# Kernel optimization log

Hardware: AMD Instinct MI355X
Metric: run time of the kernel (lower is better)

Reference implementation:

```python
import jax, jax.numpy as jnp
import numpy as np

N = 1024          # n noisy tokens (seq = 2*N)
DIM = 768
HEADS = 12
HD = DIM // HEADS
BLOCK = 16        # diffusion block size
COND = 128
DFF = 4 * DIM
NEG = -1e30


def rotate_half(x):
    x1, x2 = jnp.split(x, 2, axis=-1)
    return jnp.concatenate((-x2, x1), axis=-1)


def layernorm(x):
    mu = jnp.mean(x, axis=-1, keepdims=True)
    var = jnp.var(x, axis=-1, keepdims=True)
    return (x - mu) * jax.lax.rsqrt(var + 1e-5)


def block_diff_mask(seq, n, block_size):
    idx = jnp.arange(seq)
    q_idx, kv_idx = idx[:, None], idx[None, :]
    fq = q_idx >= n
    fk = kv_idx >= n
    bq = jnp.where(fq, (q_idx - n) // block_size, q_idx // block_size)
    bk = jnp.where(fk, (kv_idx - n) // block_size, kv_idx // block_size)
    block_diagonal = (bq == bk) & (fq == fk)
    offset_block_causal = (bq > bk) & fk & (~fq)
    block_causal = (bq >= bk) & fk & fq
    return block_diagonal | offset_block_causal | block_causal  # [seq, seq] bool


def setup_inputs() -> dict:
    key = jax.random.key(0)
    ks = jax.random.split(key, 12)
    x = jax.random.normal(ks[0], (2, 2 * N, DIM), dtype=jnp.float32)
    c = jax.random.normal(ks[1], (2, COND), dtype=jnp.float32)
    # rotary tables over positions 0..N-1 (each half of the sequence reuses them)
    inv_freq = 1.0 / (10000.0 ** (jnp.arange(0, HD, 2, dtype=jnp.float32) / HD))
    freqs = jnp.arange(N, dtype=jnp.float32)[:, None] * inv_freq[None, :]  # [N, HD/2]
    emb = jnp.concatenate((freqs, freqs), axis=-1)  # [N, HD]
    cos, sin = jnp.cos(emb), jnp.sin(emb)
    s = 0.02
    W_qkv = jax.random.normal(ks[2], (DIM, 3 * DIM), dtype=jnp.float32) * s
    W_out = jax.random.normal(ks[3], (DIM, DIM), dtype=jnp.float32) * s
    ln1_w = jnp.ones((DIM,), dtype=jnp.float32)
    ln2_w = jnp.ones((DIM,), dtype=jnp.float32)
    mlp_w1 = jax.random.normal(ks[4], (DIM, DFF), dtype=jnp.float32) * s
    mlp_b1 = jnp.zeros((DFF,), dtype=jnp.float32)
    mlp_w2 = jax.random.normal(ks[5], (DFF, DIM), dtype=jnp.float32) * s
    mlp_b2 = jnp.zeros((DIM,), dtype=jnp.float32)
    ada_w = jax.random.normal(ks[6], (COND, 6 * DIM), dtype=jnp.float32) * s
    ada_b = jax.random.normal(ks[7], (6 * DIM,), dtype=jnp.float32) * s
    return {"x": x, "cos": cos, "sin": sin, "c": c, "W_qkv": W_qkv, "W_out": W_out,
            "ln1_w": ln1_w, "ln2_w": ln2_w, "mlp_w1": mlp_w1, "mlp_b1": mlp_b1,
            "mlp_w2": mlp_w2, "mlp_b2": mlp_b2, "ada_w": ada_w, "ada_b": ada_b}


def reference(x, cos, sin, c, W_qkv, W_out, ln1_w, ln2_w,
              mlp_w1, mlp_b1, mlp_w2, mlp_b2, ada_w, ada_b):
    b, seq, dim = x.shape
    n = seq // 2
    # adaLN modulation: [b, 1, dim] each (inference: dropout = identity)
    ada = (c @ ada_w + ada_b)[:, None, :]
    shift_msa, scale_msa, gate_msa, shift_mlp, scale_mlp, gate_mlp = jnp.split(ada, 6, axis=2)
    x_skip = x
    h = layernorm(x) * ln1_w
    h = h * (1.0 + scale_msa) + shift_msa  # modulate_fused

    def qkv_rope(seg):
        qkv = (seg @ W_qkv).reshape(b, n, 3, HEADS, HD)
        cs = cos[None, :, None, None, :]
        sn = sin[None, :, None, None, :]
        return qkv * cs + rotate_half(qkv) * sn

    # noisy half and clean (x0) half each get positions 0..n-1
    qkv = jnp.concatenate((qkv_rope(h[:, :n]), qkv_rope(h[:, n:])), axis=1)  # [b,2n,3,H,HD]
    q, k, v = qkv[:, :, 0], qkv[:, :, 1], qkv[:, :, 2]  # [b, 2n, H, HD]
    mask = block_diff_mask(seq, n, BLOCK)  # [2n, 2n]
    scores = jnp.einsum('bqhd,bkhd->bhqk', q, k) / jnp.sqrt(jnp.float32(HD))
    scores = jnp.where(mask[None, None], scores, NEG)
    attn = jax.nn.softmax(scores, axis=-1)
    o = jnp.einsum('bhqk,bkhd->bqhd', attn, v).reshape(b, seq, dim)
    # bias_dropout_add_scale (inference): gate * out + residual
    x1 = gate_msa * (o @ W_out) + x_skip
    h2 = layernorm(x1) * ln2_w
    h2 = h2 * (1.0 + scale_mlp) + shift_mlp
    mlp = jax.nn.gelu(h2 @ mlp_w1 + mlp_b1, approximate=True) @ mlp_w2 + mlp_b2
    return gate_mlp * mlp + x1
```

## Files before the change

kernel.cpp:

```cpp
#include <hip/hip_runtime.h>
#include <hip/hip_bf16.h>
#include <stdint.h>

#define DIM 768
#define SEQ 2048
#define TOKENS 4096
#define HEADS 12
#define DFF 3072
#define COND 128
#define ADA6 4608

typedef __attribute__((ext_vector_type(8))) short bf16x8;
typedef __attribute__((ext_vector_type(4))) float f32x4;

#define MFMA16x32(a, b, c) __builtin_amdgcn_mfma_f32_16x16x32_bf16(a, b, c, 0, 0, 0)
#define GLDS16(g, l)                                                                  \
    __builtin_amdgcn_global_load_lds((const __attribute__((address_space(1))) void*)(g), \
                                     (__attribute__((address_space(3))) void*)(l), 16, 0, 0)

__device__ __forceinline__ ushort f2bf(float f) {
    union { float f; uint32_t u; } v;
    v.f = f;
    uint32_t r = v.u + 0x7FFF + ((v.u >> 16) & 1);
    return (ushort)(r >> 16);
}

__device__ __forceinline__ uint32_t packbf2(float a, float b) {
    union { __hip_bfloat162 h; uint32_t u; } cv;
    cv.h = __float22bfloat162_rn(make_float2(a, b));
    return cv.u;
}

__global__ void ada_kernel(const float* __restrict__ c, const float* __restrict__ ada_w,
                           const float* __restrict__ ada_b, float* __restrict__ ada) {
    int j = blockIdx.x * 256 + threadIdx.x;
    int bb = blockIdx.y;
    if (j < ADA6) {
        float acc = ada_b[j];
        for (int k = 0; k < COND; ++k)
            acc = fmaf(c[bb * COND + k], ada_w[(long)k * ADA6 + j], acc);
        ada[bb * ADA6 + j] = acc;
    }
}

__global__ __launch_bounds__(256) void convT(const float* __restrict__ W,
                                             ushort* __restrict__ Wt, int K, int N) {
    __shared__ float t[64][65];
    int tid = threadIdx.x;
    int n0 = blockIdx.x * 64, k0 = blockIdx.y * 64;
#pragma unroll
    for (int it = 0; it < 4; ++it) {
        int idx = it * 256 + tid;
        int kr = idx >> 4, nc = (idx & 15) * 4;
        float4 v = *(const float4*)&W[(long)(k0 + kr) * N + n0 + nc];
        t[kr][nc] = v.x; t[kr][nc + 1] = v.y; t[kr][nc + 2] = v.z; t[kr][nc + 3] = v.w;
    }
    __syncthreads();
#pragma unroll
    for (int it = 0; it < 4; ++it) {
        int idx = it * 256 + tid;
        int nr = idx >> 4, kc = (idx & 15) * 4;
        ushort4 v;
        v.x = f2bf(t[kc][nr]); v.y = f2bf(t[kc + 1][nr]);
        v.z = f2bf(t[kc + 2][nr]); v.w = f2bf(t[kc + 3][nr]);
        *(ushort4*)&Wt[(long)(n0 + nr) * K + k0 + kc] = v;
    }
}

__global__ __launch_bounds__(256) void ln_mod_kernel(const float* __restrict__ x,
                                                     const float* __restrict__ w,
                                                     const float* __restrict__ ada,
                                                     int shiftOff, int scaleOff,
                                                     ushort* __restrict__ out) {
    int token = blockIdx.x;
    int bb = token >> 11;
    int tid = threadIdx.x;
    const float* xi = x + (long)token * DIM;
    float v[3];
    float sum = 0.f, sumsq = 0.f;
#pragma unroll
    for (int t = 0; t < 3; ++t) {
        float val = xi[tid + 256 * t];
        v[t] = val;
        sum += val;
        sumsq = fmaf(val, val, sumsq);
    }
    for (int msk = 1; msk < 64; msk <<= 1) {
        sum += __shfl_xor(sum, msk, 64);
        sumsq += __shfl_xor(sumsq, msk, 64);
    }
    __shared__ float red0[4], red1[4];
    int wave = tid >> 6;
    if ((tid & 63) == 0) { red0[wave] = sum; red1[wave] = sumsq; }
    __syncthreads();
    sum = red0[0] + red0[1] + red0[2] + red0[3];
    sumsq = red1[0] + red1[1] + red1[2] + red1[3];
    float mu = sum * (1.f / DIM);
    float var = sumsq * (1.f / DIM) - mu * mu;
    float rs = rsqrtf(var + 1e-5f);
    const float* sh = ada + bb * ADA6 + shiftOff;
    const float* sc = ada + bb * ADA6 + scaleOff;
    ushort* oi = out + (long)token * DIM;
#pragma unroll
    for (int t = 0; t < 3; ++t) {
        int j = tid + 256 * t;
        oi[j] = f2bf((v[t] - mu) * rs * w[j] * (1.f + sc[j]) + sh[j]);
    }
}

template <int EPI, int BM>
__global__ __launch_bounds__(256) void gemm_bf16(const ushort* __restrict__ A,
                                                 const ushort* __restrict__ B,
                                                 void* __restrict__ Cp, int M, int N, int K,
                                                 const float* __restrict__ bias,
                                                 const float* __restrict__ gate,
                                                 const float* __restrict__ skip,
                                                 const float* __restrict__ cosT,
                                                 const float* __restrict__ sinT) {
    constexpr int MR = BM / 32;
    __shared__ ushort As[2][BM * 64];
    __shared__ ushort Bs[2][128 * 64];
    const int tid = threadIdx.x;
    const int wave = tid >> 6, lane = tid & 63;
    const int lo = lane & 15, hi = lane >> 4;
    const int wr = wave >> 1, wc = wave & 1;
    const int gx = gridDim.x;
    const int nwg = gx * gridDim.y;
    const int flat = blockIdx.y * gx + blockIdx.x;
    const int swzid = (flat & 7) * (nwg >> 3) + (flat >> 3);
    const int row0 = (swzid / gx) * BM, col0 = (swzid % gx) * 128;
    const int srow = tid >> 3;
    const int scol = (tid & 7) * 8;
    f32x4 acc[MR][4] = {};
    const long astep = (long)32 * K;
    const ushort* Ag = A + (long)(row0 + srow) * K + scol;
    const ushort* Bg = B + (long)(col0 + srow) * K + scol;

    auto STAGE = [&](int buf, int kt) {
        const int k0 = kt * 64;
#pragma unroll
        for (int t = 0; t < MR; ++t)
            GLDS16(Ag + t * astep + k0, (char*)As[buf] + (t * 256 + tid) * 16);
#pragma unroll
        for (int t = 0; t < 4; ++t)
            GLDS16(Bg + t * astep + k0, (char*)Bs[buf] + (t * 256 + tid) * 16);
    };

    const int nkt = K >> 6;
    STAGE(0, 0);
    for (int kt = 0; kt < nkt; ++kt) {
        const int cur = kt & 1;
        if (kt + 1 < nkt) {
            STAGE(1 - cur, kt + 1);
            if constexpr (BM == 128)
                asm volatile("s_waitcnt vmcnt(8)" ::: "memory");
            else
                asm volatile("s_waitcnt vmcnt(6)" ::: "memory");
        } else {
            asm volatile("s_waitcnt vmcnt(0)" ::: "memory");
        }
        __builtin_amdgcn_s_barrier();
        __builtin_amdgcn_sched_barrier(0);
#pragma unroll
        for (int kk = 0; kk < 2; ++kk) {
            bf16x8 af[MR], bfr[4];
#pragma unroll
            for (int m = 0; m < MR; ++m)
                af[m] = *(const bf16x8*)&As[cur][(wr * (BM / 2) + m * 16 + lo) * 64 + kk * 32 + hi * 8];
#pragma unroll
            for (int n = 0; n < 4; ++n)
                bfr[n] = *(const bf16x8*)&Bs[cur][(wc * 64 + n * 16 + lo) * 64 + kk * 32 + hi * 8];
#pragma unroll
            for (int m = 0; m < MR; ++m)
#pragma unroll
                for (int n = 0; n < 4; ++n)
                    acc[m][n] = MFMA16x32(af[m], bfr[n], acc[m][n]);
        }
        __builtin_amdgcn_s_barrier();
    }
    if (EPI == 0) {
        ushort* C = (ushort*)Cp;
#pragma unroll
        for (int m = 0; m < MR; ++m)
#pragma unroll
            for (int reg = 0; reg < 4; ++reg) {
                int r = row0 + wr * (BM / 2) + m * 16 + hi * 4 + reg;
                int pos = r & 1023;
                const float* cb = cosT + pos * 64;
                const float* sb = sinT + pos * 64;
                long rb = (long)r * N + col0 + wc * 64;
#pragma unroll
                for (int pr = 0; pr < 2; ++pr) {
                    int i = pr * 16 + lo;
                    float v0 = acc[m][pr][reg], v1 = acc[m][pr + 2][reg];
                    float c0 = cb[i], s0 = sb[i], c1 = cb[i + 32], s1 = sb[i + 32];
                    C[rb + i] = f2bf(v0 * c0 - v1 * s0);
                    C[rb + i + 32] = f2bf(v1 * c1 + v0 * s1);
                }
            }
    } else if (EPI == 1) {
        float* C = (float*)Cp;
#pragma unroll
        for (int m = 0; m < MR; ++m)
#pragma unroll
            for (int reg = 0; reg < 4; ++reg) {
                int r = row0 + wr * (BM / 2) + m * 16 + hi * 4 + reg;
                int bbi = r >> 11;
#pragma unroll
                for (int n = 0; n < 4; ++n) {
                    int c = col0 + wc * 64 + n * 16 + lo;
                    C[(long)r * N + c] =
                        gate[bbi * ADA6 + c] * acc[m][n][reg] + skip[(long)r * DIM + c];
                }
            }
    } else if (EPI == 2) {
        ushort* C = (ushort*)Cp;
#pragma unroll
        for (int m = 0; m < MR; ++m)
#pragma unroll
            for (int reg = 0; reg < 4; ++reg) {
                int r = row0 + wr * (BM / 2) + m * 16 + hi * 4 + reg;
#pragma unroll
                for (int n = 0; n < 4; ++n) {
                    int c = col0 + wc * 64 + n * 16 + lo;
                    float v = acc[m][n][reg] + bias[c];
                    float g = v / (1.f + __expf(-1.5957691216f * (v + 0.044715f * v * v * v)));
                    C[(long)r * N + c] = f2bf(g);
                }
            }
    } else {
        float* C = (float*)Cp;
#pragma unroll
        for (int m = 0; m < MR; ++m)
#pragma unroll
            for (int reg = 0; reg < 4; ++reg) {
                int r = row0 + wr * (BM / 2) + m * 16 + hi * 4 + reg;
                int bbi = r >> 11;
#pragma unroll
                for (int n = 0; n < 4; ++n) {
                    int c = col0 + wc * 64 + n * 16 + lo;
                    C[(long)r * N + c] = gate[bbi * ADA6 + c] * (acc[m][n][reg] + bias[c]) +
                                         skip[(long)r * DIM + c];
                }
            }
    }
}

__global__ __launch_bounds__(256) void vtrans(const ushort* __restrict__ qkv,
                                              ushort* __restrict__ vt) {
    __shared__ ushort t[64][65];
    int tid = threadIdx.x;
    int tb = blockIdx.x;
    int head = blockIdx.y;
    int bb = blockIdx.z;
#pragma unroll
    for (int it = 0; it < 4; ++it) {
        int idx = it * 256 + tid;
        int tok = idx >> 4, d4 = (idx & 15) * 4;
        const ushort* p = qkv + ((long)bb * SEQ + tb * 64 + tok) * 2304 + 1536 + head * 64 + d4;
        ushort4 v = *(const ushort4*)p;
        t[tok][d4] = v.x; t[tok][d4 + 1] = v.y; t[tok][d4 + 2] = v.z; t[tok][d4 + 3] = v.w;
    }
    __syncthreads();
#pragma unroll
    for (int it = 0; it < 4; ++it) {
        int idx = it * 256 + tid;
        int d = idx >> 4, t4 = (idx & 15) * 4;
        ushort4 v;
        v.x = t[t4][d]; v.y = t[t4 + 1][d]; v.z = t[t4 + 2][d]; v.w = t[t4 + 3][d];
        *(ushort4*)&vt[((long)(bb * HEADS + head) * 64 + d) * SEQ + tb * 64 + t4] = v;
    }
}

__global__ __launch_bounds__(256) void attn_mfma(const ushort* __restrict__ qkv,
                                                 const ushort* __restrict__ vt,
                                                 ushort* __restrict__ o) {
    __shared__ ushort Ks[2][4096];
    __shared__ ushort Vs[2][4096];
    __shared__ char ps[4][2048];
    const int tid = threadIdx.x;
    const int wave = tid >> 6, lane = tid & 63;
    const int lo = lane & 15, hi = lane >> 4;
    const int bx = blockIdx.x;
    const int tile = (bx & 1) ? (31 - (bx >> 1)) : (15 - (bx >> 1));
    const int head = blockIdx.y;
    const int bb = blockIdx.z;
    char* psb = ps[wave];
    const int swz = (lo & 7) << 4;
    const bool fh = tile < 16;
    const int ncausal = fh ? ((tile * 64 + 111) >> 6) : (tile - 15);
    const int nchunks = ncausal + (fh ? 1 : 0);
    const int q0 = tile * 64 + wave * 16;
    const int vcaus = fh ? q0 : (q0 - 1024 + 16);
    const long row0 = (long)bb * SEQ + q0;

    const ushort* Qp = qkv + (row0 + lo) * 2304 + head * 64 + hi * 8;
    bf16x8 qf0 = *(const bf16x8*)Qp;
    bf16x8 qf1 = *(const bf16x8*)(Qp + 32);
    f32x4 oacc[4] = {};
    float m_run = -3.0e38f, l_run = 0.f;

    const int srow = tid >> 3;
    const int sc8 = tid & 7;
    const ushort* Kg = qkv + ((long)bb * SEQ) * 2304 + DIM + head * 64;
    const ushort* Vg = vt + ((long)(bb * HEADS + head) * 64) * SEQ;

    auto STAGE = [&](int buf, int kbase) {
#pragma unroll
        for (int it = 0; it < 2; ++it) {
            int r = it * 32 + srow;
            int c8 = sc8 ^ (r & 7);
            GLDS16(Kg + (long)(kbase + r) * 2304 + c8 * 8,
                   (char*)Ks[buf] + it * 4096 + tid * 16);
        }
#pragma unroll
        for (int it = 0; it < 2; ++it) {
            int r = it * 32 + srow;
            int c8 = sc8 ^ (r & 7);
            GLDS16(Vg + (long)r * SEQ + kbase + c8 * 8,
                   (char*)Vs[buf] + it * 4096 + tid * 16);
        }
    };
#define KB(cc) (((cc) < ncausal) ? (1024 + (cc) * 64) : (tile * 64))

    STAGE(0, KB(0));
    for (int c = 0; c < nchunks; ++c) {
        const int cur = c & 1;
        if (c + 1 < nchunks) {
            STAGE(1 - cur, KB(c + 1));
            asm volatile("s_waitcnt vmcnt(4)" ::: "memory");
        } else {
            asm volatile("s_waitcnt vmcnt(0)" ::: "memory");
        }
        __builtin_amdgcn_s_barrier();
        __builtin_amdgcn_sched_barrier(0);
        const bool isdiag = (c >= ncausal);
        const int v = isdiag ? 16 : (vcaus - c * 64);
        if (v > 0) {
            f32x4 s4[4];
#pragma unroll
            for (int n = 0; n < 4; ++n) {
                f32x4 z = {};
#pragma unroll
                for (int kk = 0; kk < 2; ++kk) {
                    const bf16x8 kf = *(const bf16x8*)((const char*)Ks[cur] +
                        ((n * 16 + lo) << 7) + ((((kk << 2) + hi) ^ (lo & 7)) << 4));
                    z = MFMA16x32(kf, kk ? qf1 : qf0, z);
                }
                s4[n] = z;
            }
            const int vv = isdiag ? 64 : min(v, 64);
            float p[4][4];
            float mx = -3.0e38f;
#pragma unroll
            for (int n = 0; n < 4; ++n)
#pragma unroll
                for (int g = 0; g < 4; ++g) {
                    bool ok = isdiag ? (n == wave) : (n * 16 + hi * 4 + g < vv);
                    float val = ok ? s4[n][g] * 0.125f : -3.0e38f;
                    p[n][g] = val;
                    mx = fmaxf(mx, val);
                }
            mx = fmaxf(mx, __shfl_xor(mx, 16, 64));
            mx = fmaxf(mx, __shfl_xor(mx, 32, 64));
            float m_new = fmaxf(m_run, mx);
            float scale = __expf(m_run - m_new);
            float psum = 0.f;
#pragma unroll
            for (int n = 0; n < 4; ++n)
#pragma unroll
                for (int g = 0; g < 4; ++g) {
                    float e = __expf(p[n][g] - m_new);
                    p[n][g] = e;
                    psum += e;
                }
            psum += __shfl_xor(psum, 16, 64);
            psum += __shfl_xor(psum, 32, 64);
            l_run = l_run * scale + psum;
            m_run = m_new;
#pragma unroll
            for (int dt = 0; dt < 4; ++dt) oacc[dt] *= scale;
#pragma unroll
            for (int n = 0; n < 4; ++n)
#pragma unroll
                for (int pr = 0; pr < 2; ++pr) {
                    uint32_t u = packbf2(p[n][pr * 2], p[n][pr * 2 + 1]);
                    *(uint32_t*)(psb + lo * 128 + ((n * 32 + hi * 8 + pr * 4) ^ swz)) = u;
                }
            bf16x8 pa0 = *(const bf16x8*)(psb + lo * 128 + ((hi * 16) ^ swz));
            bf16x8 pa1 = *(const bf16x8*)(psb + lo * 128 + ((64 + hi * 16) ^ swz));
#pragma unroll
            for (int dt = 0; dt < 4; ++dt) {
#pragma unroll
                for (int kk = 0; kk < 2; ++kk) {
                    const bf16x8 vf = *(const bf16x8*)((const char*)Vs[cur] +
                        ((dt * 16 + lo) << 7) + ((((kk << 2) + hi) ^ (lo & 7)) << 4));
                    oacc[dt] = MFMA16x32(vf, kk ? pa1 : pa0, oacc[dt]);
                }
            }
        }
        __builtin_amdgcn_s_barrier();
        __builtin_amdgcn_sched_barrier(0);
    }
#undef KB

    float inv = 1.f / l_run;
#pragma unroll
    for (int dt = 0; dt < 4; ++dt) {
        ushort4 st;
        st.x = f2bf(oacc[dt][0] * inv);
        st.y = f2bf(oacc[dt][1] * inv);
        st.z = f2bf(oacc[dt][2] * inv);
        st.w = f2bf(oacc[dt][3] * inv);
        *(ushort4*)&o[(row0 + lo) * DIM + head * 64 + dt * 16 + hi * 4] = st;
    }
}

extern "C" void kernel_launch(void* const* d_in, const int* in_sizes, int n_in,
                              void* d_out, int out_size, void* d_ws, size_t ws_size,
                              hipStream_t stream) {
    const float* x      = (const float*)d_in[0];
    const float* cosT   = (const float*)d_in[1];
    const float* sinT   = (const float*)d_in[2];
    const float* c      = (const float*)d_in[3];
    const float* W_qkv  = (const float*)d_in[4];
    const float* W_out  = (const float*)d_in[5];
    const float* ln1_w  = (const float*)d_in[6];
    const float* ln2_w  = (const float*)d_in[7];
    const float* mlp_w1 = (const float*)d_in[8];
    const float* mlp_b1 = (const float*)d_in[9];
    const float* mlp_w2 = (const float*)d_in[10];
    const float* mlp_b2 = (const float*)d_in[11];
    const float* ada_w  = (const float*)d_in[12];
    const float* ada_b  = (const float*)d_in[13];
    float* out = (float*)d_out;

    char* ws = (char*)d_ws;
    float*  ada   = (float*)(ws + 0);
    ushort* h     = (ushort*)(ws + 65536L);
    ushort* qkv   = (ushort*)(ws + 6356992L);
    ushort* vt    = (ushort*)(ws + 25231360L);
    ushort* o     = (ushort*)(ws + 31522816L);
    float*  x1    = (float*)(ws + 37814272L);
    ushort* a1    = (ushort*)(ws + 50397184L);
    ushort* wqkvT = (ushort*)(ws + 75563008L);
    ushort* woutT = (ushort*)(ws + 79101952L);
    ushort* w1T   = (ushort*)(ws + 80281600L);
    ushort* w2T   = (ushort*)(ws + 85000192L);

    ada_kernel<<<dim3(18, 2), 256, 0, stream>>>(c, ada_w, ada_b, ada);
    convT<<<dim3(36, 12), 256, 0, stream>>>(W_qkv, wqkvT, 768, 2304);
    convT<<<dim3(12, 12), 256, 0, stream>>>(W_out, woutT, 768, 768);
    convT<<<dim3(48, 12), 256, 0, stream>>>(mlp_w1, w1T, 768, 3072);
    convT<<<dim3(12, 48), 256, 0, stream>>>(mlp_w2, w2T, 3072, 768);

    ln_mod_kernel<<<TOKENS, 256, 0, stream>>>(x, ln1_w, ada, 0, 768, h);
    gemm_bf16<0, 128><<<dim3(18, 32), 256, 0, stream>>>(h, wqkvT, qkv, TOKENS, 2304, 768,
                                                        nullptr, nullptr, nullptr, cosT, sinT);
    vtrans<<<dim3(32, 12, 2), 256, 0, stream>>>(qkv, vt);
    attn_mfma<<<dim3(32, 12, 2), 256, 0, stream>>>(qkv, vt, o);
    gemm_bf16<1, 64><<<dim3(6, 64), 256, 0, stream>>>(o, woutT, x1, TOKENS, 768, 768,
                                                      nullptr, ada + 1536, x, nullptr, nullptr);
    ln_mod_kernel<<<TOKENS, 256, 0, stream>>>(x1, ln2_w, ada, 2304, 3072, h);
    gemm_bf16<2, 128><<<dim3(24, 32), 256, 0, stream>>>(h, w1T, a1, TOKENS, DFF, 768,
                                                        mlp_b1, nullptr, nullptr, nullptr, nullptr);
    gemm_bf16<3, 64><<<dim3(6, 64), 256, 0, stream>>>(a1, w2T, out, TOKENS, 768, DFF,
                                                      mlp_b2, ada + 3840, x1, nullptr, nullptr);
}
```

Baseline: 319.5 us.

## Add XOR LDS swizzle to GEMM and split-K the MLP down-projection

Applies an XOR swizzle to the column chunk placement in shared-memory tiles for all bf16 GEMMs, to reduce LDS bank conflicts on the MFMA fragment reads. The final MLP GEMM (K=3072, only 384 workgroups) is split into two K halves writing fp32 partials into reused workspace, followed by a separate reduction kernel that applies bias, gate and residual. This raises parallelism for the long-K GEMM but adds partial-buffer traffic and an extra launch.

```diff
diff --git a/kernel.cpp b/kernel.cpp
--- a/kernel.cpp
+++ b/kernel.cpp
@@ -108,7 +108,7 @@
     }
 }
 
-template <int EPI, int BM>
+template <int EPI, int BM, int SPLITK = 1>
 __global__ __launch_bounds__(256) void gemm_bf16(const ushort* __restrict__ A,
                                                  const ushort* __restrict__ B,
                                                  void* __restrict__ Cp, int M, int N, int K,
@@ -130,11 +130,13 @@
     const int swzid = (flat & 7) * (nwg >> 3) + (flat >> 3);
     const int row0 = (swzid / gx) * BM, col0 = (swzid % gx) * 128;
     const int srow = tid >> 3;
-    const int scol = (tid & 7) * 8;
+    const int xscol = (((tid & 7) ^ (srow & 7)) * 8);
     f32x4 acc[MR][4] = {};
-    const long astep = (long)32 * K;
-    const ushort* Ag = A + (long)(row0 + srow) * K + scol;
-    const ushort* Bg = B + (long)(col0 + srow) * K + scol;
+    const long lda = (long)K * SPLITK;
+    const long koff = (long)blockIdx.z * K;
+    const long astep = 32 * lda;
+    const ushort* Ag = A + (long)(row0 + srow) * lda + koff + xscol;
+    const ushort* Bg = B + (long)(col0 + srow) * lda + koff + xscol;
 
     auto STAGE = [&](int buf, int kt) {
         const int k0 = kt * 64;
@@ -165,11 +167,17 @@
         for (int kk = 0; kk < 2; ++kk) {
             bf16x8 af[MR], bfr[4];
 #pragma unroll
-            for (int m = 0; m < MR; ++m)
-                af[m] = *(const bf16x8*)&As[cur][(wr * (BM / 2) + m * 16 + lo) * 64 + kk * 32 + hi * 8];
-#pragma unroll
-            for (int n = 0; n < 4; ++n)
-                bfr[n] = *(const bf16x8*)&Bs[cur][(wc * 64 + n * 16 + lo) * 64 + kk * 32 + hi * 8];
+            for (int m = 0; m < MR; ++m) {
+                const int R = wr * (BM / 2) + m * 16 + lo;
+                af[m] = *(const bf16x8*)((const char*)As[cur] + R * 128 +
+                                         ((((kk << 2) + hi) ^ (lo & 7)) << 4));
+            }
+#pragma unroll
+            for (int n = 0; n < 4; ++n) {
+                const int R = wc * 64 + n * 16 + lo;
+                bfr[n] = *(const bf16x8*)((const char*)Bs[cur] + R * 128 +
+                                          ((((kk << 2) + hi) ^ (lo & 7)) << 4));
+            }
 #pragma unroll
             for (int m = 0; m < MR; ++m)
 #pragma unroll
@@ -228,7 +236,7 @@
                     C[(long)r * N + c] = f2bf(g);
                 }
             }
-    } else {
+    } else if (EPI == 3) {
         float* C = (float*)Cp;
 #pragma unroll
         for (int m = 0; m < MR; ++m)
@@ -243,7 +251,42 @@
                                          skip[(long)r * DIM + c];
                 }
             }
-    }
+    } else {
+        float* C = (float*)Cp + (long)blockIdx.z * M * N;
+#pragma unroll
+        for (int m = 0; m < MR; ++m)
+#pragma unroll
+            for (int reg = 0; reg < 4; ++reg) {
+                int r = row0 + wr * (BM / 2) + m * 16 + hi * 4 + reg;
+#pragma unroll
+                for (int n = 0; n < 4; ++n) {
+                    int c = col0 + wc * 64 + n * 16 + lo;
+                    C[(long)r * N + c] = acc[m][n][reg];
+                }
+            }
+    }
+}
+
+__global__ __launch_bounds__(256) void splitk_red(const float* __restrict__ part,
+                                                  const float* __restrict__ bias,
+                                                  const float* __restrict__ ada,
+                                                  const float* __restrict__ skip,
+                                                  float* __restrict__ C) {
+    long i = ((long)blockIdx.x * 256 + threadIdx.x) * 4;
+    int col = (int)(i % DIM);
+    int row = (int)(i / DIM);
+    int bb = row >> 11;
+    float4 a = *(const float4*)&part[i];
+    float4 b = *(const float4*)&part[(long)TOKENS * DIM + i];
+    float4 bi = *(const float4*)&bias[col];
+    float4 g = *(const float4*)&ada[bb * ADA6 + 3840 + col];
+    float4 s = *(const float4*)&skip[i];
+    float4 r;
+    r.x = g.x * (a.x + b.x + bi.x) + s.x;
+    r.y = g.y * (a.y + b.y + bi.y) + s.y;
+    r.z = g.z * (a.z + b.z + bi.z) + s.z;
+    r.w = g.w * (a.w + b.w + bi.w) + s.w;
+    *(float4*)&C[i] = r;
 }
 
 __global__ __launch_bounds__(256) void vtrans(const ushort* __restrict__ qkv,
@@ -439,6 +482,7 @@
     float*  ada   = (float*)(ws + 0);
     ushort* h     = (ushort*)(ws + 65536L);
     ushort* qkv   = (ushort*)(ws + 6356992L);
+    float*  part  = (float*)(ws + 6356992L);
     ushort* vt    = (ushort*)(ws + 25231360L);
     ushort* o     = (ushort*)(ws + 31522816L);
     float*  x1    = (float*)(ws + 37814272L);
@@ -464,6 +508,8 @@
     ln_mod_kernel<<<TOKENS, 256, 0, stream>>>(x1, ln2_w, ada, 2304, 3072, h);
     gemm_bf16<2, 128><<<dim3(24, 32), 256, 0, stream>>>(h, w1T, a1, TOKENS, DFF, 768,
                                                         mlp_b1, nullptr, nullptr, nullptr, nullptr);
-    gemm_bf16<3, 64><<<dim3(6, 64), 256, 0, stream>>>(a1, w2T, out, TOKENS, 768, DFF,
-                                                      mlp_b2, ada + 3840, x1, nullptr, nullptr);
-}
+    gemm_bf16<4, 64, 2><<<dim3(6, 64, 2), 256, 0, stream>>>(a1, w2T, part, TOKENS, 768, 1536,
+                                                            nullptr, nullptr, nullptr, nullptr,
+                                                            nullptr);
+    splitk_red<<<3072, 256, 0, stream>>>(part, mlp_b2, ada, x1, out);
+}
```

After: 293.4 us. 1.09x faster.
